# Optimization experiments

Hardware: AMD Instinct MI355X
Metric: run time of the kernel (lower is better)

## Reference

```python
import jax, jax.numpy as jnp
import numpy as np

# ---- static skeleton topology (SMPL 24-joint kinematic tree) ----
J = 24
CIN = 32   # in_channels_per_joint
COUT = 32  # out_channels_per_joint
K = 3      # temporal kernel size
NEG_SLOPE = 0.2
ADJ_LIST = [[0,1,2,3],[1,0,4],[2,0,5],[3,0,6],[4,1,7],[5,2,8],[6,3,9],[7,4,10],[8,5,11],
            [9,6,12,13,14],[10,7],[11,8],[12,9,15],[13,9,16],[14,9,17],[15,12],[16,13,18],
            [17,14,19],[18,16,20],[19,17,21],[20,18,22],[21,19,23],[22,20],[23,21]]

# joint-level adjacency mask [J, J]
_mask_j = np.zeros((J, J), dtype=np.float32)
for i, nbrs in enumerate(ADJ_LIST):
    _mask_j[i, nbrs] = 1.0
# expand to channel-block mask [J*COUT, J*CIN, 1]
MASK = np.kron(_mask_j, np.ones((COUT, CIN), dtype=np.float32))[:, :, None]

# pooling: merge pairs of consecutive joints -> 12 regions of 2
REGIONS = np.arange(J).reshape(J // 2, 2)            # [12, 2]
R = REGIONS.shape[0]
# coarsened adjacency: region r ~ region s if any member joints are adjacent
POST_ADJ = (_mask_j.reshape(R, 2, R, 2).any(axis=(1, 3))).astype(np.int32)  # [12, 12]


def setup_inputs() -> dict:
    key = jax.random.key(0)
    k1, k2 = jax.random.split(key)
    B, T = 8, 4096
    x = jax.random.normal(k1, (B, J * CIN, T), dtype=jnp.float32)
    W = jax.random.normal(k2, (J * COUT, J * CIN, K), dtype=jnp.float32) * 0.02
    b = jnp.zeros((J * COUT,), dtype=jnp.float32)
    return {"x": x, "W": W, "b": b}


def reference(x, W, b):
    # SkeletalConv: adjacency-masked temporal conv1d (stride 1, SAME padding)
    Wm = W * jnp.asarray(MASK)
    y = jax.lax.conv_general_dilated(
        x, Wm, window_strides=(1,), padding="SAME",
        dimension_numbers=("NCW", "OIW", "NCW"))
    y = y + b[None, :, None]
    # LeakyReLU(0.2)
    y = jnp.where(y > 0, y, NEG_SLOPE * y)
    # SkeletalPooling: average channel blocks of joints within each region
    B, _, T = y.shape
    yr = y.reshape(B, J, COUT, T)              # [B, J, C, T]
    pooled = yr[:, jnp.asarray(REGIONS)]       # [B, R, 2, C, T]
    pooled = pooled.mean(axis=2).reshape(B, R * COUT, T)
    return pooled, jnp.asarray(REGIONS), jnp.asarray(POST_ADJ)
```

## Files before the change

kernel.cpp:

```cpp
#include <hip/hip_runtime.h>
#include <hip/hip_bf16.h>
#include <utility>

#define J_     24
#define CIN_   32
#define COUT_  32
#define B_     8
#define T_     4096
#define R_     12
#define TT_    128
#define POOLED_SZ_ (B_ * R_ * COUT_ * T_)
#define XT_ELEMS_  ((size_t)B_ * T_ * (J_ * CIN_))
#define NFRAG_     420
#define BSLAB_     9216
#define ALDS_      49152

typedef float  f32x4  __attribute__((ext_vector_type(4)));
typedef short  bf16x8 __attribute__((ext_vector_type(8)));
typedef unsigned short us8 __attribute__((ext_vector_type(8)));

static constexpr unsigned kAdjMask[J_] = {
    0x0000000Fu, 0x00000013u, 0x00000025u, 0x00000049u, 0x00000092u, 0x00000124u,
    0x00000248u, 0x00000490u, 0x00000920u, 0x00007240u, 0x00000480u, 0x00000900u,
    0x00009200u, 0x00012200u, 0x00024200u, 0x00009000u, 0x00052000u, 0x000A4000u,
    0x00150000u, 0x002A0000u, 0x00540000u, 0x00A80000u, 0x00500000u, 0x00A00000u
};
static constexpr int kAdjOff[J_ + 1] = {
    0,4,7,10,13,16,19,22,25,28,33,35,37,40,43,46,48,51,54,57,60,63,66,68,70
};
static constexpr int edge_of(int jout, int nb) {
    return kAdjOff[jout] + __builtin_popcount(kAdjMask[jout] & ((1u << nb) - 1u));
}
static constexpr int nedges(int j) { return kAdjOff[j + 1] - kAdjOff[j]; }
static constexpr int local_base(int RGN, int js, int nb) {
    const int j = 2 * RGN + js;
    const int within = edge_of(j, nb) - kAdjOff[j];
    const int pre = js ? nedges(2 * RGN) : 0;
    return (pre + within) * 6;
}
static constexpr unsigned union_mask(int r) { return kAdjMask[2 * r] | kAdjMask[2 * r + 1]; }
static constexpr int union_rank(int r, int nb) {
    return __builtin_popcount(union_mask(r) & ((1u << nb) - 1u));
}

__device__ __constant__ unsigned int ADJMASK[J_] = {
    0x0000000Fu, 0x00000013u, 0x00000025u, 0x00000049u, 0x00000092u, 0x00000124u,
    0x00000248u, 0x00000490u, 0x00000920u, 0x00007240u, 0x00000480u, 0x00000900u,
    0x00009200u, 0x00012200u, 0x00024200u, 0x00009000u, 0x00052000u, 0x000A4000u,
    0x00150000u, 0x002A0000u, 0x00540000u, 0x00A80000u, 0x00500000u, 0x00A00000u
};
__device__ __constant__ int ADJ_FLAT[70] = {
    0,1,2,3,  0,1,4,  0,2,5,  0,3,6,  1,4,7,  2,5,8,  3,6,9,  4,7,10,  5,8,11,
    6,9,12,13,14,  7,10,  8,11,  9,12,15,  9,13,16,  9,14,17,  12,15,
    13,16,18,  14,17,19,  16,18,20,  17,19,21,  18,20,22,  19,21,23,  20,22,  21,23
};
__device__ __constant__ int ADJ_OFF[J_ + 1] = {
    0,4,7,10,13,16,19,22,25,28,33,35,37,40,43,46,48,51,54,57,60,63,66,68,70
};
__device__ __constant__ int UNION_CNT[R_] = {5,5,6,6,8,4,5,5,6,6,6,4};
__device__ __constant__ int UNION_NB[R_][8] = {
    {0,1,2,3,4,0,0,0},      {0,2,3,5,6,0,0,0},      {1,2,4,5,7,8,0,0},
    {3,4,6,7,9,10,0,0},     {5,6,8,9,11,12,13,14},  {7,8,10,11,0,0,0,0},
    {9,12,13,15,16,0,0,0},  {9,12,14,15,17,0,0,0},  {13,14,16,17,18,19,0,0},
    {16,17,18,19,20,21,0,0},{18,19,20,21,22,23,0,0},{20,21,22,23,0,0,0,0}
};

static __device__ __forceinline__ unsigned short f2bf(float f) {
    unsigned u = __float_as_uint(f);
    unsigned r = (u + 0x7fffu + ((u >> 16) & 1u)) >> 16;
    return (unsigned short)r;
}

static __device__ __forceinline__ void gload_lds16(const void* g, void* l) {
    __builtin_amdgcn_global_load_lds(
        (const __attribute__((address_space(1))) unsigned int*)g,
        (__attribute__((address_space(3))) unsigned int*)l, 16, 0, 0);
}

__global__ __launch_bounds__(256)
void skel_transpose(const float* __restrict__ x, unsigned short* __restrict__ xT)
{
    __shared__ float xs[32][257];
    const int tid = threadIdx.x;
    const int tt0 = blockIdx.x * 256;
    const int cg  = blockIdx.y;
    const int b   = blockIdx.z;

    const float* xp = x + ((size_t)b * (J_ * CIN_) + cg * 32) * T_ + tt0;
#pragma unroll
    for (int i = 0; i < 8; ++i) {
        const int idx = tid + i * 256;
        const int row = idx >> 6;
        const int c4  = (idx & 63) << 2;
        const float4 v = *(const float4*)(xp + (size_t)row * T_ + c4);
        xs[row][c4 + 0] = v.x; xs[row][c4 + 1] = v.y;
        xs[row][c4 + 2] = v.z; xs[row][c4 + 3] = v.w;
    }
    __syncthreads();

    union { unsigned short u[32]; uint4 q[4]; } pk;
#pragma unroll
    for (int c = 0; c < 32; ++c) pk.u[c] = f2bf(xs[c][tid]);
    unsigned short* dst = xT + ((size_t)b * T_ + tt0 + tid) * (J_ * CIN_) + cg * 32;
#pragma unroll
    for (int k = 0; k < 4; ++k) *(uint4*)(dst + k * 8) = pk.q[k];
}

__global__ __launch_bounds__(64)
void skel_pack(const float* __restrict__ W, unsigned short* __restrict__ wsW,
               float* __restrict__ out_regions, float* __restrict__ out_post)
{
    const int fb = blockIdx.x;
    const int l  = threadIdx.x;
    if (fb == NFRAG_) {
        for (int i = l; i < J_; i += 64) out_regions[i] = (float)i;
        for (int i = l; i < R_ * R_; i += 64) {
            const int r1 = i / R_, r2 = i - r1 * R_;
            const unsigned m = ADJMASK[2 * r1] | ADJMASK[2 * r1 + 1];
            out_post[i] = ((m >> (2 * r2)) & 3u) ? 1.0f : 0.0f;
        }
        return;
    }
    const int cot = fb & 1;
    const int tmp = fb >> 1;
    const int kw  = tmp % 3;
    const int e   = tmp / 3;
    int jout = 0;
    while (ADJ_OFF[jout + 1] <= e) ++jout;
    const int nb = ADJ_FLAT[e];
    const int co = cot * 16 + (l & 15);
    const int hi = l >> 4;

    union { unsigned short u[8]; uint4 q; } pk;
#pragma unroll
    for (int j = 0; j < 8; ++j) {
        const int ci = hi * 8 + j;
        const float w = W[((size_t)(jout * COUT_ + co) * (J_ * CIN_) + (nb * CIN_ + ci)) * 3 + kw];
        pk.u[j] = f2bf(w);
    }
    *(uint4*)(wsW + (size_t)fb * 512 + l * 8) = pk.q;
}

template<int RGN, int NB>
__device__ __forceinline__ void nb_step(const unsigned char* __restrict__ ldsB,
                                        const unsigned short* __restrict__ ldsl,
                                        int rtb, int hi, f32x4 acc[2][2])
{
    constexpr bool e0 = (kAdjMask[2 * RGN] >> NB) & 1u;
    constexpr bool e1 = (kAdjMask[2 * RGN + 1] >> NB) & 1u;
    if constexpr (!(e0 || e1)) return;

    constexpr int SLAB = union_rank(RGN, NB);
    const unsigned char* bbase = ldsB + SLAB * BSLAB_;

    bf16x8 bfr[3];
#pragma unroll
    for (int kw = 0; kw < 3; ++kw) {
        const int rt = rtb + kw;
        bfr[kw] = *(const bf16x8*)(bbase + rt * 64 + ((hi ^ (rt & 3)) << 4));
    }
    if constexpr (e0) {
        constexpr int LB = local_base(RGN, 0, NB);
#pragma unroll
        for (int kw = 0; kw < 3; ++kw)
#pragma unroll
            for (int cot = 0; cot < 2; ++cot) {
                const bf16x8 a = *(const bf16x8*)(ldsl + (size_t)(LB + kw * 2 + cot) * 512);
                acc[0][cot] = __builtin_amdgcn_mfma_f32_16x16x32_bf16(
                    a, bfr[kw], acc[0][cot], 0, 0, 0);
            }
    }
    if constexpr (e1) {
        constexpr int LB = local_base(RGN, 1, NB);
#pragma unroll
        for (int kw = 0; kw < 3; ++kw)
#pragma unroll
            for (int cot = 0; cot < 2; ++cot) {
                const bf16x8 a = *(const bf16x8*)(ldsl + (size_t)(LB + kw * 2 + cot) * 512);
                acc[1][cot] = __builtin_amdgcn_mfma_f32_16x16x32_bf16(
                    a, bfr[kw], acc[1][cot], 0, 0, 0);
            }
    }
}

template<int RGN, int... NBs>
__device__ __forceinline__ void region_all(std::integer_sequence<int, NBs...>,
                                           const unsigned char* __restrict__ ldsB,
                                           const unsigned short* __restrict__ ldsl,
                                           int rtb, int hi, f32x4 acc[2][2])
{
    (nb_step<RGN, NBs>(ldsB, ldsl, rtb, hi, acc), ...);
}

__global__ __launch_bounds__(512, 2)
void skel_main(const unsigned short* __restrict__ xT,
               const unsigned short* __restrict__ wsW,
               const float* __restrict__ bias, float* __restrict__ out)
{
    const int i    = blockIdx.x;
    const int xcd  = i & 7;
    const int slot = i >> 3;
    const int r    = slot % R_;
    const int gi   = slot / R_;
    const int g    = xcd + 8 * gi;
    const int b    = g >> 5;
    const int t0   = (g & 31) * TT_;

    const int tid  = threadIdx.x;
    const int wv   = tid >> 6;
    const int lane = tid & 63;
    const int l15  = lane & 15;
    const int hi   = lane >> 4;

    __shared__ __align__(16) unsigned char lds[ALDS_ + 8 * BSLAB_];
    unsigned short* ldsA = (unsigned short*)lds;
    unsigned char*  ldsB = lds + ALDS_;

    const int j0 = 2 * r, j1 = 2 * r + 1;

    {
        const int NU = UNION_CNT[r];
        if (wv < NU) {
            const int nb = UNION_NB[r][wv];
            const unsigned short* gb = xT + (size_t)b * T_ * (J_ * CIN_) + nb * CIN_;
            unsigned char* ldst = ldsB + wv * BSLAB_;
            const int lrow = lane >> 2, lslot = lane & 3;
#pragma unroll
            for (int L = 0; L < 9; ++L) {
                const int rt = L * 16 + lrow;
                int t = t0 - 1 + rt;
                t = t < 0 ? 0 : (t > T_ - 1 ? T_ - 1 : t);
                const unsigned short* gsrc = gb + (size_t)t * (J_ * CIN_)
                                             + ((lslot ^ (rt & 3)) << 3);
                gload_lds16(gsrc, ldst + L * 1024);
            }
        }
    }
    {
        const int n0 = ADJ_OFF[j0 + 1] - ADJ_OFF[j0];
        const int n1 = ADJ_OFF[j1 + 1] - ADJ_OFF[j1];
        const uint4* s0 = (const uint4*)(wsW + (size_t)ADJ_OFF[j0] * 6 * 512);
        const uint4* s1 = (const uint4*)(wsW + (size_t)ADJ_OFF[j1] * 6 * 512);
        uint4* dA = (uint4*)ldsA;
        const int q0 = n0 * 384;
        const int q1 = n1 * 384;
        for (int c = tid; c < q0; c += 512) dA[c] = s0[c];
        for (int c = tid; c < q1; c += 512) dA[q0 + c] = s1[c];
    }
    __syncthreads();

    if (t0 == 0 || t0 == T_ - TT_) {
        const int zr = (t0 == 0) ? 0 : (TT_ + 1);
        if (tid < 32) {
            const uint4 z = {0u, 0u, 0u, 0u};
            *(uint4*)(ldsB + (tid >> 2) * BSLAB_ + zr * 64 + (tid & 3) * 16) = z;
        }
        __syncthreads();
    }

    f32x4 acc[2][2];
#pragma unroll
    for (int a = 0; a < 2; ++a)
#pragma unroll
        for (int c = 0; c < 2; ++c) acc[a][c] = (f32x4){0.f, 0.f, 0.f, 0.f};

    const unsigned short* ldsl = ldsA + lane * 8;
    const int rtb = wv * 16 + l15;

    using Seq = std::make_integer_sequence<int, J_>;
    switch (r) {
        case 0:  region_all<0>(Seq{}, ldsB, ldsl, rtb, hi, acc); break;
        case 1:  region_all<1>(Seq{}, ldsB, ldsl, rtb, hi, acc); break;
        case 2:  region_all<2>(Seq{}, ldsB, ldsl, rtb, hi, acc); break;
        case 3:  region_all<3>(Seq{}, ldsB, ldsl, rtb, hi, acc); break;
        case 4:  region_all<4>(Seq{}, ldsB, ldsl, rtb, hi, acc); break;
        case 5:  region_all<5>(Seq{}, ldsB, ldsl, rtb, hi, acc); break;
        case 6:  region_all<6>(Seq{}, ldsB, ldsl, rtb, hi, acc); break;
        case 7:  region_all<7>(Seq{}, ldsB, ldsl, rtb, hi, acc); break;
        case 8:  region_all<8>(Seq{}, ldsB, ldsl, rtb, hi, acc); break;
        case 9:  region_all<9>(Seq{}, ldsB, ldsl, rtb, hi, acc); break;
        case 10: region_all<10>(Seq{}, ldsB, ldsl, rtb, hi, acc); break;
        default: region_all<11>(Seq{}, ldsB, ldsl, rtb, hi, acc); break;
    }

#pragma unroll
    for (int cot = 0; cot < 2; ++cot) {
#pragma unroll
        for (int q = 0; q < 4; ++q) {
            const int co  = cot * 16 + hi * 4 + q;
            float y0 = acc[0][cot][q] + bias[j0 * COUT_ + co];
            y0 = (y0 > 0.f) ? y0 : 0.2f * y0;
            float y1 = acc[1][cot][q] + bias[j1 * COUT_ + co];
            y1 = (y1 > 0.f) ? y1 : 0.2f * y1;
            out[((size_t)b * (R_ * COUT_) + r * COUT_ + co) * T_
                + t0 + wv * 16 + l15] = 0.5f * (y0 + y1);
        }
    }
}

extern "C" void kernel_launch(void* const* d_in, const int* in_sizes, int n_in,
                              void* d_out, int out_size, void* d_ws, size_t ws_size,
                              hipStream_t stream)
{
    const float* x    = (const float*)d_in[0];
    const float* W    = (const float*)d_in[1];
    const float* bias = (const float*)d_in[2];
    float* out = (float*)d_out;

    unsigned short* xT  = (unsigned short*)d_ws;
    unsigned short* wsW = xT + XT_ELEMS_;

    dim3 tgrid(T_ / 256, J_ * CIN_ / 32, B_);
    skel_transpose<<<tgrid, 256, 0, stream>>>(x, xT);

    float* out_regions = out + POOLED_SZ_;
    float* out_post    = out_regions + J_;
    skel_pack<<<NFRAG_ + 1, 64, 0, stream>>>(W, wsW, out_regions, out_post);

    skel_main<<<(T_ / TT_) * R_ * B_, 512, 0, stream>>>(xT, wsW, bias, out);
}
```

Before: 84.54 us.

## Switch to 32x32x16 MFMA with per-joint wave split and LDS pooling reduction

Replaces the 16x16x32 bf16 MFMA tiling, where every wave computed both joints of a region over 16 time steps, with 32x32x16 MFMAs. Each wave now handles one joint over 32 time steps, and the weight pack layout is changed to match the new operand fragments. The two joints' results are combined through an LDS scratch exchange with extra barriers before the pooled store. The aim is fewer, larger MFMAs and less redundant B-fragment loading. The cost is a 16-float accumulator, extra syncs, half the waves idle during the store, and dropping the occupancy hint of 2 from launch bounds.

```diff
diff --git a/kernel.cpp b/kernel.cpp
--- a/kernel.cpp
+++ b/kernel.cpp
@@ -16,6 +16,7 @@
 #define ALDS_      49152
 
 typedef float  f32x4  __attribute__((ext_vector_type(4)));
+typedef float  f32x16 __attribute__((ext_vector_type(16)));
 typedef short  bf16x8 __attribute__((ext_vector_type(8)));
 typedef unsigned short us8 __attribute__((ext_vector_type(8)));
 
@@ -121,78 +122,71 @@
         }
         return;
     }
-    const int cot = fb & 1;
+    const int h   = fb & 1;
     const int tmp = fb >> 1;
     const int kw  = tmp % 3;
     const int e   = tmp / 3;
     int jout = 0;
     while (ADJ_OFF[jout + 1] <= e) ++jout;
     const int nb = ADJ_FLAT[e];
-    const int co = cot * 16 + (l & 15);
-    const int hi = l >> 4;
+    const int co = l & 31;
+    const int g2 = l >> 5;
 
     union { unsigned short u[8]; uint4 q; } pk;
 #pragma unroll
     for (int j = 0; j < 8; ++j) {
-        const int ci = hi * 8 + j;
+        const int ci = h * 16 + g2 * 8 + j;
         const float w = W[((size_t)(jout * COUT_ + co) * (J_ * CIN_) + (nb * CIN_ + ci)) * 3 + kw];
         pk.u[j] = f2bf(w);
     }
     *(uint4*)(wsW + (size_t)fb * 512 + l * 8) = pk.q;
 }
 
-template<int RGN, int NB>
+template<int RGN, int JS, int NB>
 __device__ __forceinline__ void nb_step(const unsigned char* __restrict__ ldsB,
                                         const unsigned short* __restrict__ ldsl,
-                                        int rtb, int hi, f32x4 acc[2][2])
-{
-    constexpr bool e0 = (kAdjMask[2 * RGN] >> NB) & 1u;
-    constexpr bool e1 = (kAdjMask[2 * RGN + 1] >> NB) & 1u;
-    if constexpr (!(e0 || e1)) return;
-
+                                        int rtb, int g2, f32x16& acc)
+{
+    constexpr bool e_ = (kAdjMask[2 * RGN + JS] >> NB) & 1u;
+    if constexpr (!e_) return;
     constexpr int SLAB = union_rank(RGN, NB);
+    constexpr int LB   = local_base(RGN, JS, NB);
     const unsigned char* bbase = ldsB + SLAB * BSLAB_;
 
-    bf16x8 bfr[3];
 #pragma unroll
     for (int kw = 0; kw < 3; ++kw) {
         const int rt = rtb + kw;
-        bfr[kw] = *(const bf16x8*)(bbase + rt * 64 + ((hi ^ (rt & 3)) << 4));
-    }
-    if constexpr (e0) {
-        constexpr int LB = local_base(RGN, 0, NB);
-#pragma unroll
-        for (int kw = 0; kw < 3; ++kw)
-#pragma unroll
-            for (int cot = 0; cot < 2; ++cot) {
-                const bf16x8 a = *(const bf16x8*)(ldsl + (size_t)(LB + kw * 2 + cot) * 512);
-                acc[0][cot] = __builtin_amdgcn_mfma_f32_16x16x32_bf16(
-                    a, bfr[kw], acc[0][cot], 0, 0, 0);
-            }
-    }
-    if constexpr (e1) {
-        constexpr int LB = local_base(RGN, 1, NB);
-#pragma unroll
-        for (int kw = 0; kw < 3; ++kw)
-#pragma unroll
-            for (int cot = 0; cot < 2; ++cot) {
-                const bf16x8 a = *(const bf16x8*)(ldsl + (size_t)(LB + kw * 2 + cot) * 512);
-                acc[1][cot] = __builtin_amdgcn_mfma_f32_16x16x32_bf16(
-                    a, bfr[kw], acc[1][cot], 0, 0, 0);
-            }
-    }
-}
-
-template<int RGN, int... NBs>
-__device__ __forceinline__ void region_all(std::integer_sequence<int, NBs...>,
+#pragma unroll
+        for (int h = 0; h < 2; ++h) {
+            const int s = 2 * h + g2;
+            const bf16x8 bv = *(const bf16x8*)(bbase + rt * 64 + ((s ^ (rt & 3)) << 4));
+            const bf16x8 a  = *(const bf16x8*)(ldsl + (size_t)(LB + kw * 2 + h) * 512);
+            acc = __builtin_amdgcn_mfma_f32_32x32x16_bf16(a, bv, acc, 0, 0, 0);
+        }
+    }
+}
+
+template<int RGN, int JS, int... NBs>
+__device__ __forceinline__ void joint_all(std::integer_sequence<int, NBs...>,
+                                          const unsigned char* __restrict__ ldsB,
+                                          const unsigned short* __restrict__ ldsl,
+                                          int rtb, int g2, f32x16& acc)
+{
+    (nb_step<RGN, JS, NBs>(ldsB, ldsl, rtb, g2, acc), ...);
+}
+
+template<int RGN>
+__device__ __forceinline__ void run_region(int js,
                                            const unsigned char* __restrict__ ldsB,
                                            const unsigned short* __restrict__ ldsl,
-                                           int rtb, int hi, f32x4 acc[2][2])
-{
-    (nb_step<RGN, NBs>(ldsB, ldsl, rtb, hi, acc), ...);
-}
-
-__global__ __launch_bounds__(512, 2)
+                                           int rtb, int g2, f32x16& acc)
+{
+    using Seq = std::make_integer_sequence<int, J_>;
+    if (js == 0) joint_all<RGN, 0>(Seq{}, ldsB, ldsl, rtb, g2, acc);
+    else         joint_all<RGN, 1>(Seq{}, ldsB, ldsl, rtb, g2, acc);
+}
+
+__global__ __launch_bounds__(512)
 void skel_main(const unsigned short* __restrict__ xT,
                const unsigned short* __restrict__ wsW,
                const float* __restrict__ bias, float* __restrict__ out)
@@ -209,8 +203,10 @@
     const int tid  = threadIdx.x;
     const int wv   = tid >> 6;
     const int lane = tid & 63;
-    const int l15  = lane & 15;
-    const int hi   = lane >> 4;
+    const int l31  = lane & 31;
+    const int g2   = lane >> 5;
+    const int ws   = wv & 3;
+    const int js   = wv >> 2;
 
     __shared__ __align__(16) unsigned char lds[ALDS_ + 8 * BSLAB_];
     unsigned short* ldsA = (unsigned short*)lds;
@@ -258,42 +254,58 @@
         __syncthreads();
     }
 
-    f32x4 acc[2][2];
-#pragma unroll
-    for (int a = 0; a < 2; ++a)
-#pragma unroll
-        for (int c = 0; c < 2; ++c) acc[a][c] = (f32x4){0.f, 0.f, 0.f, 0.f};
+    f32x16 acc;
+#pragma unroll
+    for (int q = 0; q < 16; ++q) acc[q] = 0.0f;
 
     const unsigned short* ldsl = ldsA + lane * 8;
-    const int rtb = wv * 16 + l15;
-
-    using Seq = std::make_integer_sequence<int, J_>;
+    const int rtb = ws * 32 + l31;
+
     switch (r) {
-        case 0:  region_all<0>(Seq{}, ldsB, ldsl, rtb, hi, acc); break;
-        case 1:  region_all<1>(Seq{}, ldsB, ldsl, rtb, hi, acc); break;
-        case 2:  region_all<2>(Seq{}, ldsB, ldsl, rtb, hi, acc); break;
-        case 3:  region_all<3>(Seq{}, ldsB, ldsl, rtb, hi, acc); break;
-        case 4:  region_all<4>(Seq{}, ldsB, ldsl, rtb, hi, acc); break;
-        case 5:  region_all<5>(Seq{}, ldsB, ldsl, rtb, hi, acc); break;
-        case 6:  region_all<6>(Seq{}, ldsB, ldsl, rtb, hi, acc); break;
-        case 7:  region_all<7>(Seq{}, ldsB, ldsl, rtb, hi, acc); break;
-        case 8:  region_all<8>(Seq{}, ldsB, ldsl, rtb, hi, acc); break;
-        case 9:  region_all<9>(Seq{}, ldsB, ldsl, rtb, hi, acc); break;
-        case 10: region_all<10>(Seq{}, ldsB, ldsl, rtb, hi, acc); break;
-        default: region_all<11>(Seq{}, ldsB, ldsl, rtb, hi, acc); break;
-    }
-
-#pragma unroll
-    for (int cot = 0; cot < 2; ++cot) {
-#pragma unroll
-        for (int q = 0; q < 4; ++q) {
-            const int co  = cot * 16 + hi * 4 + q;
-            float y0 = acc[0][cot][q] + bias[j0 * COUT_ + co];
-            y0 = (y0 > 0.f) ? y0 : 0.2f * y0;
-            float y1 = acc[1][cot][q] + bias[j1 * COUT_ + co];
-            y1 = (y1 > 0.f) ? y1 : 0.2f * y1;
-            out[((size_t)b * (R_ * COUT_) + r * COUT_ + co) * T_
-                + t0 + wv * 16 + l15] = 0.5f * (y0 + y1);
+        case 0:  run_region<0>(js, ldsB, ldsl, rtb, g2, acc); break;
+        case 1:  run_region<1>(js, ldsB, ldsl, rtb, g2, acc); break;
+        case 2:  run_region<2>(js, ldsB, ldsl, rtb, g2, acc); break;
+        case 3:  run_region<3>(js, ldsB, ldsl, rtb, g2, acc); break;
+        case 4:  run_region<4>(js, ldsB, ldsl, rtb, g2, acc); break;
+        case 5:  run_region<5>(js, ldsB, ldsl, rtb, g2, acc); break;
+        case 6:  run_region<6>(js, ldsB, ldsl, rtb, g2, acc); break;
+        case 7:  run_region<7>(js, ldsB, ldsl, rtb, g2, acc); break;
+        case 8:  run_region<8>(js, ldsB, ldsl, rtb, g2, acc); break;
+        case 9:  run_region<9>(js, ldsB, ldsl, rtb, g2, acc); break;
+        case 10: run_region<10>(js, ldsB, ldsl, rtb, g2, acc); break;
+        default: run_region<11>(js, ldsB, ldsl, rtb, g2, acc); break;
+    }
+
+    const int jw = 2 * r + js;
+    f32x4 yv[4];
+#pragma unroll
+    for (int qq = 0; qq < 4; ++qq) {
+#pragma unroll
+        for (int qi = 0; qi < 4; ++qi) {
+            const int co = 8 * qq + 4 * g2 + qi;
+            float y = acc[qq * 4 + qi] + bias[jw * COUT_ + co];
+            yv[qq][qi] = (y > 0.f) ? y : 0.2f * y;
+        }
+    }
+
+    __syncthreads();
+    float* scr = (float*)lds;
+    if (js == 1) {
+#pragma unroll
+        for (int qq = 0; qq < 4; ++qq)
+            *(f32x4*)(scr + ws * 4096 + qq * 1024 + lane * 4) = yv[qq];
+    }
+    __syncthreads();
+    if (js == 0) {
+#pragma unroll
+        for (int qq = 0; qq < 4; ++qq) {
+            const f32x4 pv = *(const f32x4*)(scr + ws * 4096 + qq * 1024 + lane * 4);
+#pragma unroll
+            for (int qi = 0; qi < 4; ++qi) {
+                const int co = 8 * qq + 4 * g2 + qi;
+                out[((size_t)b * (R_ * COUT_) + r * COUT_ + co) * T_
+                    + t0 + ws * 32 + l31] = 0.5f * (yv[qq][qi] + pv[qi]);
+            }
         }
     }
 }
```

Result: slower. 92.91 us (+9.9%).
